# Optimization experiments

Hardware: AMD Instinct MI355X
Metric: run time of the kernel (lower is better)

The kernel has to match this reference:

```python
import jax, jax.numpy as jnp
import numpy as np

NUM_EMBEDDINGS = 512
EMBEDDING_DIM = 64
COMMITMENT_COST = 0.25


def setup_inputs() -> dict:
    key = jax.random.key(0)
    kx, kc = jax.random.split(key)
    x = jax.random.normal(kx, (32, 64, 64, EMBEDDING_DIM), dtype=jnp.float32)
    # nn.Embedding weight initialized uniform(-1/K, 1/K)
    codebook = jax.random.uniform(
        kc, (NUM_EMBEDDINGS, EMBEDDING_DIM), dtype=jnp.float32,
        minval=-1.0 / NUM_EMBEDDINGS, maxval=1.0 / NUM_EMBEDDINGS)
    return {"x": x, "codebook": codebook}


def reference(x, codebook):
    D = codebook.shape[1]
    flat = x.reshape(-1, D)  # [N, D]
    # squared euclidean distances; argmin is identical to cdist(p=2) argmin
    d2 = (jnp.sum(flat * flat, axis=-1, keepdims=True)
          - 2.0 * (flat @ codebook.T)
          + jnp.sum(codebook * codebook, axis=-1))  # [N, K]
    idx = jnp.argmin(d2, axis=1)  # [N]
    quantized = codebook[idx].reshape(x.shape)  # gather == one-hot @ codebook
    e_latent_loss = jnp.mean((jax.lax.stop_gradient(quantized) - x) ** 2)
    q_latent_loss = jnp.mean((quantized - jax.lax.stop_gradient(x)) ** 2)
    loss = q_latent_loss + COMMITMENT_COST * e_latent_loss
    # straight-through estimator
    quantized_st = x + jax.lax.stop_gradient(quantized - x)
    return quantized_st, loss
```

## Files before the change

kernel.cpp:

```cpp
#include <hip/hip_runtime.h>

#define DIMS 64
#define KCB 512
#define OUT_Q 8388608
#define MAIN_WGS 512

typedef float f32x4 __attribute__((ext_vector_type(4)));
typedef float f4    __attribute__((ext_vector_type(4)));
typedef short short8 __attribute__((ext_vector_type(8)));


static __device__ __forceinline__ unsigned int f2bf(float f) {
    unsigned int u = __float_as_uint(f);
    unsigned int r = u + 0x7FFFu + ((u >> 16) & 1u);
    return r >> 16;
}

__global__ void vq_prep(const float* __restrict__ cb, float* __restrict__ ws) {
    int t = blockIdx.x * blockDim.x + threadIdx.x;
    if (t < 4096) {
        int kt = t >> 7, rest = t & 127;
        int h = rest >> 6, l = rest & 63;
        int row = kt * 16 + (l & 15);
        int col = h * 32 + ((l >> 4) & 3) * 8;
        const f4* p = (const f4*)(cb + row * DIMS + col);
        f4 u0 = p[0], u1 = p[1];
        unsigned int* dst = (unsigned int*)((char*)ws + 4096 + kt * 2048 + h * 1024 + l * 16);
        dst[0] = (f2bf(u0[1]) << 16) | f2bf(u0[0]);
        dst[1] = (f2bf(u0[3]) << 16) | f2bf(u0[2]);
        dst[2] = (f2bf(u1[1]) << 16) | f2bf(u1[0]);
        dst[3] = (f2bf(u1[3]) << 16) | f2bf(u1[2]);
    } else if (t < 4096 + KCB) {
        int r = t - 4096;
        const f4* p = (const f4*)(cb + r * DIMS);
        float s = 0.0f;
#pragma unroll
        for (int i = 0; i < DIMS / 4; ++i) {
            f4 v = p[i];
            s += v[0]*v[0] + v[1]*v[1] + v[2]*v[2] + v[3]*v[3];
        }
        ws[512 + r] = -0.5f * s;
    }
}

__global__ __launch_bounds__(512, 4) void vq_main(const float* __restrict__ x,
                                                  const float* __restrict__ cb,
                                                  float* __restrict__ out,
                                                  float* __restrict__ ws) {
    __shared__ char lds[66560];

    const int tid  = threadIdx.x;
    const int lane = tid & 63;
    const int wid  = tid >> 6;
    const int wave = blockIdx.x * 8 + wid;
    const long rowbase = (long)wave * 32;
    const int r15 = lane & 15;
    const int g   = lane >> 4;

    {
        const f4* src = (const f4*)((const char*)ws + 4096);
        f4* ldsv = (f4*)lds;
#pragma unroll
        for (int r = 0; r < 8; ++r)
            ldsv[r * 512 + tid] = src[r * 512 + tid];
        ((float*)(lds + 65536))[tid] = ws[512 + tid];
    }

    short8 A00, A01, A10, A11;
    float xn0 = 0.0f, xn1 = 0.0f;
    {
        const float* xa = x + (rowbase + r15) * DIMS + g * 8;
#define LOADA(FR, OFF, XN)                                                     \
        {                                                                      \
            const f4* p_ = (const f4*)(xa + (OFF));                            \
            f4 a_ = p_[0], b_ = p_[1];                                         \
            XN += a_[0]*a_[0] + a_[1]*a_[1] + a_[2]*a_[2] + a_[3]*a_[3]        \
                + b_[0]*b_[0] + b_[1]*b_[1] + b_[2]*b_[2] + b_[3]*b_[3];       \
            union { unsigned int u[4]; short8 s; } q_;                         \
            asm("v_cvt_pk_bf16_f32 %0, %1, %2" : "=v"(q_.u[0]) : "v"(a_[0]), "v"(a_[1])); \
            asm("v_cvt_pk_bf16_f32 %0, %1, %2" : "=v"(q_.u[1]) : "v"(a_[2]), "v"(a_[3])); \
            asm("v_cvt_pk_bf16_f32 %0, %1, %2" : "=v"(q_.u[2]) : "v"(b_[0]), "v"(b_[1])); \
            asm("v_cvt_pk_bf16_f32 %0, %1, %2" : "=v"(q_.u[3]) : "v"(b_[2]), "v"(b_[3])); \
            FR = q_.s;                                                         \
        }
        LOADA(A00, 0, xn0)
        LOADA(A01, 32, xn0)
        LOADA(A10, 16 * DIMS, xn1)
        LOADA(A11, 16 * DIMS + 32, xn1)
#undef LOADA
    }
    xn0 += __shfl_xor(xn0, 16, 64);  xn0 += __shfl_xor(xn0, 32, 64);
    xn1 += __shfl_xor(xn1, 16, 64);  xn1 += __shfl_xor(xn1, 32, 64);

    __syncthreads();

    float bv00 = -3.4e38f, bv01 = -3.4e38f, bv02 = -3.4e38f, bv03 = -3.4e38f;
    float bv10 = -3.4e38f, bv11 = -3.4e38f, bv12 = -3.4e38f, bv13 = -3.4e38f;

    const char*  ldsb = lds;
    const float* ldsn = (const float*)(lds + 65536);
    const int laneoff = lane * 16;

#define PKMAX(BV, S)                                                           \
    BV = fmaxf(BV, __uint_as_float((__float_as_uint(S) & 0xFFFFFE00u) | kr));

#pragma unroll
    for (int kt = 0; kt < 32; ++kt) {
        short8 b0 = *(const short8*)(ldsb + kt * 2048 + laneoff);
        short8 b1 = *(const short8*)(ldsb + kt * 2048 + 1024 + laneoff);
        float ic = ldsn[kt * 16 + r15];
        f32x4 init = {ic, ic, ic, ic};
        f32x4 a0 = __builtin_amdgcn_mfma_f32_16x16x32_bf16(A00, b0, init, 0, 0, 0);
        a0       = __builtin_amdgcn_mfma_f32_16x16x32_bf16(A01, b1, a0,  0, 0, 0);
        f32x4 a1 = __builtin_amdgcn_mfma_f32_16x16x32_bf16(A10, b0, init, 0, 0, 0);
        a1       = __builtin_amdgcn_mfma_f32_16x16x32_bf16(A11, b1, a1,  0, 0, 0);
        const unsigned int kr = (unsigned int)(kt * 16 + r15);
        PKMAX(bv00, a0[0]) PKMAX(bv01, a0[1]) PKMAX(bv02, a0[2]) PKMAX(bv03, a0[3])
        PKMAX(bv10, a1[0]) PKMAX(bv11, a1[1]) PKMAX(bv12, a1[2]) PKMAX(bv13, a1[3])
    }
#undef PKMAX

#pragma unroll
    for (int st = 0; st < 4; ++st) {
        const int m = 1 << st;
        bv00 = fmaxf(bv00, __shfl_xor(bv00, m, 64));
        bv01 = fmaxf(bv01, __shfl_xor(bv01, m, 64));
        bv02 = fmaxf(bv02, __shfl_xor(bv02, m, 64));
        bv03 = fmaxf(bv03, __shfl_xor(bv03, m, 64));
        bv10 = fmaxf(bv10, __shfl_xor(bv10, m, 64));
        bv11 = fmaxf(bv11, __shfl_xor(bv11, m, 64));
        bv12 = fmaxf(bv12, __shfl_xor(bv12, m, 64));
        bv13 = fmaxf(bv13, __shfl_xor(bv13, m, 64));
    }

    const int orow = lane >> 2;
    const int cseg = lane & 3;
    const int j2   = orow & 3;
    int idx0 = (int)(__float_as_uint(j2 == 0 ? bv00 : j2 == 1 ? bv01 : j2 == 2 ? bv02 : bv03) & 511u);
    int idx1 = (int)(__float_as_uint(j2 == 0 ? bv10 : j2 == 1 ? bv11 : j2 == 2 ? bv12 : bv13) & 511u);

#define EPI(IDX, TOFF)                                                     \
    {                                                                      \
        const long row_ = rowbase + (TOFF) + orow;                         \
        const f4* cq_ = (const f4*)(cb + (long)(IDX) * DIMS + cseg * 16);  \
        f4* op_      = (f4*)(out + row_ * DIMS + cseg * 16);               \
        _Pragma("unroll")                                                  \
        for (int u = 0; u < 4; ++u) op_[u] = cq_[u];                       \
    }
    EPI(idx0, 0)
    EPI(idx1, 16)
#undef EPI

    float lsum = 0.0f;
    if (g == (r15 >> 2)) {
        const int jp = r15 & 3;
        float s0 = jp == 0 ? bv00 : jp == 1 ? bv01 : jp == 2 ? bv02 : bv03;
        float s1 = jp == 0 ? bv10 : jp == 1 ? bv11 : jp == 2 ? bv12 : bv13;
        s0 = __uint_as_float(__float_as_uint(s0) & 0xFFFFFE00u);
        s1 = __uint_as_float(__float_as_uint(s1) & 0xFFFFFE00u);
        lsum = (xn0 - 2.0f * s0) + (xn1 - 2.0f * s1);
    }
#pragma unroll
    for (int s = 0; s < 6; ++s) lsum += __shfl_xor(lsum, 1 << s, 64);

    __syncthreads();
    float* lsred = (float*)lds;
    if (lane == 0) lsred[wid] = lsum;
    __syncthreads();
    if (tid == 0) {
        ws[blockIdx.x] = lsred[0] + lsred[1] + lsred[2] + lsred[3]
                       + lsred[4] + lsred[5] + lsred[6] + lsred[7];
    }
}

__global__ __launch_bounds__(256) void vq_final(const float* __restrict__ ws,
                                                float* __restrict__ out) {
    const int t = threadIdx.x;
    float s = ws[t] + ws[t + 256];
#pragma unroll
    for (int st = 0; st < 6; ++st) s += __shfl_xor(s, 1 << st, 64);
    __shared__ float w2[4];
    if ((t & 63) == 0) w2[t >> 6] = s;
    __syncthreads();
    if (t == 0) {
        float total = w2[0] + w2[1] + w2[2] + w2[3];
        out[OUT_Q] = 1.25f * total / 8388608.0f;
    }
}

extern "C" void kernel_launch(void* const* d_in, const int* in_sizes, int n_in,
                              void* d_out, int out_size, void* d_ws, size_t ws_size,
                              hipStream_t stream) {
    const float* x  = (const float*)d_in[0];
    const float* cb = (const float*)d_in[1];
    float* out = (float*)d_out;
    float* ws  = (float*)d_ws;
    vq_prep<<<18, 256, 0, stream>>>(cb, ws);
    vq_main<<<MAIN_WGS, 512, 0, stream>>>(x, cb, out, ws);
    vq_final<<<1, 256, 0, stream>>>(ws, out);
}
```

Before: 31.53 us.

## Fuse codebook prep into main kernel and process 64 rows per wave

Drops the separate prep kernel. Each workgroup now converts the codebook to bf16 MFMA layout and computes its norms directly into LDS. Workgroups shrink to 256 threads, and each wave handles 64 rows with four MFMA tiles instead of two, so the grid stays at 512 blocks. This saves a launch and the workspace round trip, and gets more MFMA work out of each LDS B-fragment load. In exchange, every block redoes the codebook conversion from global memory, and register pressure rises.

```diff
diff --git a/kernel.cpp b/kernel.cpp
--- a/kernel.cpp
+++ b/kernel.cpp
@@ -3,7 +3,6 @@
 #define DIMS 64
 #define KCB 512
 #define OUT_Q 8388608
-#define MAIN_WGS 512
 
 typedef float f32x4 __attribute__((ext_vector_type(4)));
 typedef float f4    __attribute__((ext_vector_type(4)));
@@ -16,58 +15,22 @@
     return r >> 16;
 }
 
-__global__ void vq_prep(const float* __restrict__ cb, float* __restrict__ ws) {
-    int t = blockIdx.x * blockDim.x + threadIdx.x;
-    if (t < 4096) {
-        int kt = t >> 7, rest = t & 127;
-        int h = rest >> 6, l = rest & 63;
-        int row = kt * 16 + (l & 15);
-        int col = h * 32 + ((l >> 4) & 3) * 8;
-        const f4* p = (const f4*)(cb + row * DIMS + col);
-        f4 u0 = p[0], u1 = p[1];
-        unsigned int* dst = (unsigned int*)((char*)ws + 4096 + kt * 2048 + h * 1024 + l * 16);
-        dst[0] = (f2bf(u0[1]) << 16) | f2bf(u0[0]);
-        dst[1] = (f2bf(u0[3]) << 16) | f2bf(u0[2]);
-        dst[2] = (f2bf(u1[1]) << 16) | f2bf(u1[0]);
-        dst[3] = (f2bf(u1[3]) << 16) | f2bf(u1[2]);
-    } else if (t < 4096 + KCB) {
-        int r = t - 4096;
-        const f4* p = (const f4*)(cb + r * DIMS);
-        float s = 0.0f;
-#pragma unroll
-        for (int i = 0; i < DIMS / 4; ++i) {
-            f4 v = p[i];
-            s += v[0]*v[0] + v[1]*v[1] + v[2]*v[2] + v[3]*v[3];
-        }
-        ws[512 + r] = -0.5f * s;
-    }
-}
-
-__global__ __launch_bounds__(512, 4) void vq_main(const float* __restrict__ x,
+__global__ __launch_bounds__(256, 2) void vq_main(const float* __restrict__ x,
                                                   const float* __restrict__ cb,
                                                   float* __restrict__ out,
                                                   float* __restrict__ ws) {
-    __shared__ char lds[66560];
+    __shared__ f4 ldsv[4224];
 
     const int tid  = threadIdx.x;
     const int lane = tid & 63;
     const int wid  = tid >> 6;
-    const int wave = blockIdx.x * 8 + wid;
-    const long rowbase = (long)wave * 32;
+    const int wave = blockIdx.x * 4 + wid;
+    const long rowbase = (long)wave * 64;
     const int r15 = lane & 15;
     const int g   = lane >> 4;
 
-    {
-        const f4* src = (const f4*)((const char*)ws + 4096);
-        f4* ldsv = (f4*)lds;
-#pragma unroll
-        for (int r = 0; r < 8; ++r)
-            ldsv[r * 512 + tid] = src[r * 512 + tid];
-        ((float*)(lds + 65536))[tid] = ws[512 + tid];
-    }
-
-    short8 A00, A01, A10, A11;
-    float xn0 = 0.0f, xn1 = 0.0f;
+    short8 A00, A01, A10, A11, A20, A21, A30, A31;
+    float xn0 = 0.0f, xn1 = 0.0f, xn2 = 0.0f, xn3 = 0.0f;
     {
         const float* xa = x + (rowbase + r15) * DIMS + g * 8;
 #define LOADA(FR, OFF, XN)                                                     \
@@ -87,18 +50,58 @@
         LOADA(A01, 32, xn0)
         LOADA(A10, 16 * DIMS, xn1)
         LOADA(A11, 16 * DIMS + 32, xn1)
+        LOADA(A20, 32 * DIMS, xn2)
+        LOADA(A21, 32 * DIMS + 32, xn2)
+        LOADA(A30, 48 * DIMS, xn3)
+        LOADA(A31, 48 * DIMS + 32, xn3)
 #undef LOADA
     }
     xn0 += __shfl_xor(xn0, 16, 64);  xn0 += __shfl_xor(xn0, 32, 64);
     xn1 += __shfl_xor(xn1, 16, 64);  xn1 += __shfl_xor(xn1, 32, 64);
+    xn2 += __shfl_xor(xn2, 16, 64);  xn2 += __shfl_xor(xn2, 32, 64);
+    xn3 += __shfl_xor(xn3, 16, 64);  xn3 += __shfl_xor(xn3, 32, 64);
+
+    {
+#pragma unroll
+        for (int i = 0; i < 16; ++i) {
+            const int s = tid + i * 256;
+            const int kt = s >> 7, rest = s & 127;
+            const int h = rest >> 6, l = rest & 63;
+            const int row = kt * 16 + (l & 15);
+            const int col = h * 32 + ((l >> 4) & 3) * 8;
+            const f4* p = (const f4*)(cb + row * DIMS + col);
+            f4 u0 = p[0], u1 = p[1];
+            union { unsigned int u[4]; f4 f; } q;
+            q.u[0] = (f2bf(u0[1]) << 16) | f2bf(u0[0]);
+            q.u[1] = (f2bf(u0[3]) << 16) | f2bf(u0[2]);
+            q.u[2] = (f2bf(u1[1]) << 16) | f2bf(u1[0]);
+            q.u[3] = (f2bf(u1[3]) << 16) | f2bf(u1[2]);
+            ldsv[s] = q.f;
+        }
+        float* ldsn_w = (float*)ldsv + 16384;
+#pragma unroll
+        for (int rr = 0; rr < 2; ++rr) {
+            const int r = tid + rr * 256;
+            const f4* p = (const f4*)(cb + r * DIMS);
+            float s0 = 0.0f;
+#pragma unroll
+            for (int i = 0; i < 16; ++i) {
+                f4 v = p[i];
+                s0 += v[0]*v[0] + v[1]*v[1] + v[2]*v[2] + v[3]*v[3];
+            }
+            ldsn_w[r] = -0.5f * s0;
+        }
+    }
 
     __syncthreads();
 
     float bv00 = -3.4e38f, bv01 = -3.4e38f, bv02 = -3.4e38f, bv03 = -3.4e38f;
     float bv10 = -3.4e38f, bv11 = -3.4e38f, bv12 = -3.4e38f, bv13 = -3.4e38f;
-
-    const char*  ldsb = lds;
-    const float* ldsn = (const float*)(lds + 65536);
+    float bv20 = -3.4e38f, bv21 = -3.4e38f, bv22 = -3.4e38f, bv23 = -3.4e38f;
+    float bv30 = -3.4e38f, bv31 = -3.4e38f, bv32 = -3.4e38f, bv33 = -3.4e38f;
+
+    const char*  ldsb = (const char*)ldsv;
+    const float* ldsn = (const float*)ldsv + 16384;
     const int laneoff = lane * 16;
 
 #define PKMAX(BV, S)                                                           \
@@ -114,9 +117,15 @@
         a0       = __builtin_amdgcn_mfma_f32_16x16x32_bf16(A01, b1, a0,  0, 0, 0);
         f32x4 a1 = __builtin_amdgcn_mfma_f32_16x16x32_bf16(A10, b0, init, 0, 0, 0);
         a1       = __builtin_amdgcn_mfma_f32_16x16x32_bf16(A11, b1, a1,  0, 0, 0);
+        f32x4 a2 = __builtin_amdgcn_mfma_f32_16x16x32_bf16(A20, b0, init, 0, 0, 0);
+        a2       = __builtin_amdgcn_mfma_f32_16x16x32_bf16(A21, b1, a2,  0, 0, 0);
+        f32x4 a3 = __builtin_amdgcn_mfma_f32_16x16x32_bf16(A30, b0, init, 0, 0, 0);
+        a3       = __builtin_amdgcn_mfma_f32_16x16x32_bf16(A31, b1, a3,  0, 0, 0);
         const unsigned int kr = (unsigned int)(kt * 16 + r15);
         PKMAX(bv00, a0[0]) PKMAX(bv01, a0[1]) PKMAX(bv02, a0[2]) PKMAX(bv03, a0[3])
         PKMAX(bv10, a1[0]) PKMAX(bv11, a1[1]) PKMAX(bv12, a1[2]) PKMAX(bv13, a1[3])
+        PKMAX(bv20, a2[0]) PKMAX(bv21, a2[1]) PKMAX(bv22, a2[2]) PKMAX(bv23, a2[3])
+        PKMAX(bv30, a3[0]) PKMAX(bv31, a3[1]) PKMAX(bv32, a3[2]) PKMAX(bv33, a3[3])
     }
 #undef PKMAX
 
@@ -131,13 +140,26 @@
         bv11 = fmaxf(bv11, __shfl_xor(bv11, m, 64));
         bv12 = fmaxf(bv12, __shfl_xor(bv12, m, 64));
         bv13 = fmaxf(bv13, __shfl_xor(bv13, m, 64));
+        bv20 = fmaxf(bv20, __shfl_xor(bv20, m, 64));
+        bv21 = fmaxf(bv21, __shfl_xor(bv21, m, 64));
+        bv22 = fmaxf(bv22, __shfl_xor(bv22, m, 64));
+        bv23 = fmaxf(bv23, __shfl_xor(bv23, m, 64));
+        bv30 = fmaxf(bv30, __shfl_xor(bv30, m, 64));
+        bv31 = fmaxf(bv31, __shfl_xor(bv31, m, 64));
+        bv32 = fmaxf(bv32, __shfl_xor(bv32, m, 64));
+        bv33 = fmaxf(bv33, __shfl_xor(bv33, m, 64));
     }
 
     const int orow = lane >> 2;
     const int cseg = lane & 3;
     const int j2   = orow & 3;
-    int idx0 = (int)(__float_as_uint(j2 == 0 ? bv00 : j2 == 1 ? bv01 : j2 == 2 ? bv02 : bv03) & 511u);
-    int idx1 = (int)(__float_as_uint(j2 == 0 ? bv10 : j2 == 1 ? bv11 : j2 == 2 ? bv12 : bv13) & 511u);
+#define SEL(T) (int)(__float_as_uint(j2 == 0 ? bv##T##0 : j2 == 1 ? bv##T##1 : \
+                                     j2 == 2 ? bv##T##2 : bv##T##3) & 511u)
+    const int idx0 = SEL(0);
+    const int idx1 = SEL(1);
+    const int idx2 = SEL(2);
+    const int idx3 = SEL(3);
+#undef SEL
 
 #define EPI(IDX, TOFF)                                                     \
     {                                                                      \
@@ -149,27 +171,28 @@
     }
     EPI(idx0, 0)
     EPI(idx1, 16)
+    EPI(idx2, 32)
+    EPI(idx3, 48)
 #undef EPI
 
     float lsum = 0.0f;
     if (g == (r15 >> 2)) {
         const int jp = r15 & 3;
-        float s0 = jp == 0 ? bv00 : jp == 1 ? bv01 : jp == 2 ? bv02 : bv03;
-        float s1 = jp == 0 ? bv10 : jp == 1 ? bv11 : jp == 2 ? bv12 : bv13;
-        s0 = __uint_as_float(__float_as_uint(s0) & 0xFFFFFE00u);
-        s1 = __uint_as_float(__float_as_uint(s1) & 0xFFFFFE00u);
-        lsum = (xn0 - 2.0f * s0) + (xn1 - 2.0f * s1);
+#define SSEL(T) __uint_as_float(__float_as_uint(jp == 0 ? bv##T##0 : jp == 1 ? bv##T##1 : \
+                                jp == 2 ? bv##T##2 : bv##T##3) & 0xFFFFFE00u)
+        lsum = (xn0 - 2.0f * SSEL(0)) + (xn1 - 2.0f * SSEL(1))
+             + (xn2 - 2.0f * SSEL(2)) + (xn3 - 2.0f * SSEL(3));
+#undef SSEL
     }
 #pragma unroll
     for (int s = 0; s < 6; ++s) lsum += __shfl_xor(lsum, 1 << s, 64);
 
     __syncthreads();
-    float* lsred = (float*)lds;
+    float* lsred = (float*)ldsv;
     if (lane == 0) lsred[wid] = lsum;
     __syncthreads();
     if (tid == 0) {
-        ws[blockIdx.x] = lsred[0] + lsred[1] + lsred[2] + lsred[3]
-                       + lsred[4] + lsred[5] + lsred[6] + lsred[7];
+        ws[blockIdx.x] = lsred[0] + lsred[1] + lsred[2] + lsred[3];
     }
 }
 
@@ -195,7 +218,6 @@
     const float* cb = (const float*)d_in[1];
     float* out = (float*)d_out;
     float* ws  = (float*)d_ws;
-    vq_prep<<<18, 256, 0, stream>>>(cb, ws);
-    vq_main<<<MAIN_WGS, 512, 0, stream>>>(x, cb, out, ws);
+    vq_main<<<512, 256, 0, stream>>>(x, cb, out, ws);
     vq_final<<<1, 256, 0, stream>>>(ws, out);
 }
```

New measurement: 42.77 us. +35.6%, slower.

## Fuse codebook prep into main kernel, building bf16 tiles in LDS per block

Applied to the files above, without the earlier changes.

Drops the separate prep kernel that converted the codebook to a bf16 MFMA layout and computed the norms. Each workgroup of the main kernel now reads the fp32 codebook, converts it and computes the norms straight into LDS, which removes one launch and the round trip through the workspace. In exchange every one of the 512 blocks repeats the conversion and norm work (extra ALU and L2 reads of the codebook). The occupancy hint moves to the waves-per-EU attribute.

```diff
diff --git a/kernel.cpp b/kernel.cpp
--- a/kernel.cpp
+++ b/kernel.cpp
@@ -16,38 +16,13 @@
     return r >> 16;
 }
 
-__global__ void vq_prep(const float* __restrict__ cb, float* __restrict__ ws) {
-    int t = blockIdx.x * blockDim.x + threadIdx.x;
-    if (t < 4096) {
-        int kt = t >> 7, rest = t & 127;
-        int h = rest >> 6, l = rest & 63;
-        int row = kt * 16 + (l & 15);
-        int col = h * 32 + ((l >> 4) & 3) * 8;
-        const f4* p = (const f4*)(cb + row * DIMS + col);
-        f4 u0 = p[0], u1 = p[1];
-        unsigned int* dst = (unsigned int*)((char*)ws + 4096 + kt * 2048 + h * 1024 + l * 16);
-        dst[0] = (f2bf(u0[1]) << 16) | f2bf(u0[0]);
-        dst[1] = (f2bf(u0[3]) << 16) | f2bf(u0[2]);
-        dst[2] = (f2bf(u1[1]) << 16) | f2bf(u1[0]);
-        dst[3] = (f2bf(u1[3]) << 16) | f2bf(u1[2]);
-    } else if (t < 4096 + KCB) {
-        int r = t - 4096;
-        const f4* p = (const f4*)(cb + r * DIMS);
-        float s = 0.0f;
-#pragma unroll
-        for (int i = 0; i < DIMS / 4; ++i) {
-            f4 v = p[i];
-            s += v[0]*v[0] + v[1]*v[1] + v[2]*v[2] + v[3]*v[3];
-        }
-        ws[512 + r] = -0.5f * s;
-    }
-}
-
-__global__ __launch_bounds__(512, 4) void vq_main(const float* __restrict__ x,
-                                                  const float* __restrict__ cb,
-                                                  float* __restrict__ out,
-                                                  float* __restrict__ ws) {
-    __shared__ char lds[66560];
+__global__ __launch_bounds__(512)
+__attribute__((amdgpu_waves_per_eu(4, 4)))
+void vq_main(const float* __restrict__ x,
+             const float* __restrict__ cb,
+             float* __restrict__ out,
+             float* __restrict__ ws) {
+    __shared__ f4 ldsv[4224];
 
     const int tid  = threadIdx.x;
     const int lane = tid & 63;
@@ -56,15 +31,6 @@
     const long rowbase = (long)wave * 32;
     const int r15 = lane & 15;
     const int g   = lane >> 4;
-
-    {
-        const f4* src = (const f4*)((const char*)ws + 4096);
-        f4* ldsv = (f4*)lds;
-#pragma unroll
-        for (int r = 0; r < 8; ++r)
-            ldsv[r * 512 + tid] = src[r * 512 + tid];
-        ((float*)(lds + 65536))[tid] = ws[512 + tid];
-    }
 
     short8 A00, A01, A10, A11;
     float xn0 = 0.0f, xn1 = 0.0f;
@@ -92,13 +58,41 @@
     xn0 += __shfl_xor(xn0, 16, 64);  xn0 += __shfl_xor(xn0, 32, 64);
     xn1 += __shfl_xor(xn1, 16, 64);  xn1 += __shfl_xor(xn1, 32, 64);
 
+    {
+#pragma unroll
+        for (int i = 0; i < 8; ++i) {
+            const int s = tid + i * 512;
+            const int kt = s >> 7, rest = s & 127;
+            const int h = rest >> 6, l = rest & 63;
+            const int row = kt * 16 + (l & 15);
+            const int col = h * 32 + ((l >> 4) & 3) * 8;
+            const f4* p = (const f4*)(cb + row * DIMS + col);
+            f4 u0 = p[0], u1 = p[1];
+            union { unsigned int u[4]; f4 f; } q;
+            q.u[0] = (f2bf(u0[1]) << 16) | f2bf(u0[0]);
+            q.u[1] = (f2bf(u0[3]) << 16) | f2bf(u0[2]);
+            q.u[2] = (f2bf(u1[1]) << 16) | f2bf(u1[0]);
+            q.u[3] = (f2bf(u1[3]) << 16) | f2bf(u1[2]);
+            ldsv[s] = q.f;
+        }
+        float* ldsn_w = (float*)ldsv + 16384;
+        const f4* p = (const f4*)(cb + tid * DIMS);
+        float s0 = 0.0f;
+#pragma unroll
+        for (int i = 0; i < 16; ++i) {
+            f4 v = p[i];
+            s0 += v[0]*v[0] + v[1]*v[1] + v[2]*v[2] + v[3]*v[3];
+        }
+        ldsn_w[tid] = -0.5f * s0;
+    }
+
     __syncthreads();
 
     float bv00 = -3.4e38f, bv01 = -3.4e38f, bv02 = -3.4e38f, bv03 = -3.4e38f;
     float bv10 = -3.4e38f, bv11 = -3.4e38f, bv12 = -3.4e38f, bv13 = -3.4e38f;
 
-    const char*  ldsb = lds;
-    const float* ldsn = (const float*)(lds + 65536);
+    const char*  ldsb = (const char*)ldsv;
+    const float* ldsn = (const float*)ldsv + 16384;
     const int laneoff = lane * 16;
 
 #define PKMAX(BV, S)                                                           \
@@ -154,17 +148,16 @@
     float lsum = 0.0f;
     if (g == (r15 >> 2)) {
         const int jp = r15 & 3;
-        float s0 = jp == 0 ? bv00 : jp == 1 ? bv01 : jp == 2 ? bv02 : bv03;
-        float s1 = jp == 0 ? bv10 : jp == 1 ? bv11 : jp == 2 ? bv12 : bv13;
-        s0 = __uint_as_float(__float_as_uint(s0) & 0xFFFFFE00u);
-        s1 = __uint_as_float(__float_as_uint(s1) & 0xFFFFFE00u);
-        lsum = (xn0 - 2.0f * s0) + (xn1 - 2.0f * s1);
+#define SSEL(T) __uint_as_float(__float_as_uint(jp == 0 ? bv##T##0 : jp == 1 ? bv##T##1 : \
+                                jp == 2 ? bv##T##2 : bv##T##3) & 0xFFFFFE00u)
+        lsum = (xn0 - 2.0f * SSEL(0)) + (xn1 - 2.0f * SSEL(1));
+#undef SSEL
     }
 #pragma unroll
     for (int s = 0; s < 6; ++s) lsum += __shfl_xor(lsum, 1 << s, 64);
 
     __syncthreads();
-    float* lsred = (float*)lds;
+    float* lsred = (float*)ldsv;
     if (lane == 0) lsred[wid] = lsum;
     __syncthreads();
     if (tid == 0) {
@@ -195,7 +188,6 @@
     const float* cb = (const float*)d_in[1];
     float* out = (float*)d_out;
     float* ws  = (float*)d_ws;
-    vq_prep<<<18, 256, 0, stream>>>(cb, ws);
     vq_main<<<MAIN_WGS, 512, 0, stream>>>(x, cb, out, ws);
     vq_final<<<1, 256, 0, stream>>>(ws, out);
 }
```

Result: slower. 40.99 us (+30.0%).

## Switch distance GEMM to FP8 MFMA and halve rows per wave

Applied to the files above, without the earlier changes.

The codebook is pre-quantized to FP8 with a scale of 256 and x is converted with v_cvt_pk_fp8_f32, so the distance matmul runs on 16x16x32 fp8 MFMA instead of bf16. This halves the LDS footprint of the codebook. Each wave now handles 16 rows instead of 32, with 1024 workgroups and launch bounds raised for higher occupancy, and the final reduction is widened to match. FP8 precision in the argmin can select different codebook entries than the fp32 reference, so the results risk mismatches in the indices and the loss.

```diff
diff --git a/kernel.cpp b/kernel.cpp
--- a/kernel.cpp
+++ b/kernel.cpp
@@ -3,17 +3,37 @@
 #define DIMS 64
 #define KCB 512
 #define OUT_Q 8388608
-#define MAIN_WGS 512
+#define MAIN_WGS 1024
 
 typedef float f32x4 __attribute__((ext_vector_type(4)));
 typedef float f4    __attribute__((ext_vector_type(4)));
-typedef short short8 __attribute__((ext_vector_type(8)));
-
-
-static __device__ __forceinline__ unsigned int f2bf(float f) {
+
+
+static __device__ __forceinline__ unsigned int f2fp8(float f) {
     unsigned int u = __float_as_uint(f);
-    unsigned int r = u + 0x7FFFu + ((u >> 16) & 1u);
-    return r >> 16;
+    unsigned int sign = (u >> 24) & 0x80u;
+    if ((u & 0x7FFFFFFFu) == 0) return sign;
+    int exp = (int)((u >> 23) & 0xFFu) - 127;
+    unsigned int m24 = (u & 0x7FFFFFu) | 0x800000u;
+    if (exp >= -6) {
+        unsigned int keep = m24 >> 20;
+        unsigned int rem = m24 & 0xFFFFFu;
+        if (rem > 0x80000u || (rem == 0x80000u && (keep & 1u))) keep++;
+        if (keep >= 16u) { keep >>= 1; exp++; }
+        int e = exp + 7;
+        if (e >= 16) return sign | 0x7Eu;
+        if (e == 15 && (keep & 7u) == 7u) return sign | 0x7Eu;
+        return sign | ((unsigned)e << 3) | (keep & 7u);
+    } else {
+        int sh = 14 - exp;
+        if (sh > 31) return sign;
+        unsigned int keep = m24 >> sh;
+        unsigned int rem = m24 & ((1u << sh) - 1u);
+        unsigned int half = 1u << (sh - 1);
+        if (rem > half || (rem == half && (keep & 1u))) keep++;
+        if (keep >= 8u) return sign | 0x08u;
+        return sign | keep;
+    }
 }
 
 __global__ void vq_prep(const float* __restrict__ cb, float* __restrict__ ws) {
@@ -25,11 +45,17 @@
         int col = h * 32 + ((l >> 4) & 3) * 8;
         const f4* p = (const f4*)(cb + row * DIMS + col);
         f4 u0 = p[0], u1 = p[1];
-        unsigned int* dst = (unsigned int*)((char*)ws + 4096 + kt * 2048 + h * 1024 + l * 16);
-        dst[0] = (f2bf(u0[1]) << 16) | f2bf(u0[0]);
-        dst[1] = (f2bf(u0[3]) << 16) | f2bf(u0[2]);
-        dst[2] = (f2bf(u1[1]) << 16) | f2bf(u1[0]);
-        dst[3] = (f2bf(u1[3]) << 16) | f2bf(u1[2]);
+        unsigned int lo = f2fp8(256.0f * u0[0])
+                        | (f2fp8(256.0f * u0[1]) << 8)
+                        | (f2fp8(256.0f * u0[2]) << 16)
+                        | (f2fp8(256.0f * u0[3]) << 24);
+        unsigned int hi = f2fp8(256.0f * u1[0])
+                        | (f2fp8(256.0f * u1[1]) << 8)
+                        | (f2fp8(256.0f * u1[2]) << 16)
+                        | (f2fp8(256.0f * u1[3]) << 24);
+        unsigned int* dst = (unsigned int*)((char*)ws + 8192 + kt * 1024 + h * 512 + l * 8);
+        dst[0] = lo;
+        dst[1] = hi;
     } else if (t < 4096 + KCB) {
         int r = t - 4096;
         const f4* p = (const f4*)(cb + r * DIMS);
@@ -39,126 +65,118 @@
             f4 v = p[i];
             s += v[0]*v[0] + v[1]*v[1] + v[2]*v[2] + v[3]*v[3];
         }
-        ws[512 + r] = -0.5f * s;
-    }
-}
-
-__global__ __launch_bounds__(512, 4) void vq_main(const float* __restrict__ x,
+        ((float*)((char*)ws + 4096))[r] = -128.0f * s;
+    }
+}
+
+__global__ __launch_bounds__(512, 8) void vq_main(const float* __restrict__ x,
                                                   const float* __restrict__ cb,
                                                   float* __restrict__ out,
                                                   float* __restrict__ ws) {
-    __shared__ char lds[66560];
+    __shared__ char lds[34816];
 
     const int tid  = threadIdx.x;
     const int lane = tid & 63;
     const int wid  = tid >> 6;
-    const int wave = blockIdx.x * 8 + wid;
-    const long rowbase = (long)wave * 32;
+    const long rowbase = ((long)blockIdx.x * 8 + wid) * 16;
     const int r15 = lane & 15;
     const int g   = lane >> 4;
 
     {
-        const f4* src = (const f4*)((const char*)ws + 4096);
-        f4* ldsv = (f4*)lds;
-#pragma unroll
-        for (int r = 0; r < 8; ++r)
-            ldsv[r * 512 + tid] = src[r * 512 + tid];
-        ((float*)(lds + 65536))[tid] = ws[512 + tid];
-    }
-
-    short8 A00, A01, A10, A11;
-    float xn0 = 0.0f, xn1 = 0.0f;
+        const f4* src = (const f4*)((const char*)ws + 8192);
+        f4 s0 = src[tid];
+        f4 s1 = src[512 + tid];
+        f4 s2 = src[1024 + tid];
+        f4 s3 = src[1536 + tid];
+        float nv = ((const float*)((const char*)ws + 4096))[tid];
+        f4* dst = (f4*)lds;
+        dst[tid]        = s0;
+        dst[512 + tid]  = s1;
+        dst[1024 + tid] = s2;
+        dst[1536 + tid] = s3;
+        ((float*)(lds + 32768))[tid] = nv;
+    }
+
+    unsigned long A0, A1;
+    float xn0;
     {
         const float* xa = x + (rowbase + r15) * DIMS + g * 8;
-#define LOADA(FR, OFF, XN)                                                     \
-        {                                                                      \
-            const f4* p_ = (const f4*)(xa + (OFF));                            \
-            f4 a_ = p_[0], b_ = p_[1];                                         \
-            XN += a_[0]*a_[0] + a_[1]*a_[1] + a_[2]*a_[2] + a_[3]*a_[3]        \
-                + b_[0]*b_[0] + b_[1]*b_[1] + b_[2]*b_[2] + b_[3]*b_[3];       \
-            union { unsigned int u[4]; short8 s; } q_;                         \
-            asm("v_cvt_pk_bf16_f32 %0, %1, %2" : "=v"(q_.u[0]) : "v"(a_[0]), "v"(a_[1])); \
-            asm("v_cvt_pk_bf16_f32 %0, %1, %2" : "=v"(q_.u[1]) : "v"(a_[2]), "v"(a_[3])); \
-            asm("v_cvt_pk_bf16_f32 %0, %1, %2" : "=v"(q_.u[2]) : "v"(b_[0]), "v"(b_[1])); \
-            asm("v_cvt_pk_bf16_f32 %0, %1, %2" : "=v"(q_.u[3]) : "v"(b_[2]), "v"(b_[3])); \
-            FR = q_.s;                                                         \
-        }
-        LOADA(A00, 0, xn0)
-        LOADA(A01, 32, xn0)
-        LOADA(A10, 16 * DIMS, xn1)
-        LOADA(A11, 16 * DIMS + 32, xn1)
-#undef LOADA
-    }
-    xn0 += __shfl_xor(xn0, 16, 64);  xn0 += __shfl_xor(xn0, 32, 64);
-    xn1 += __shfl_xor(xn1, 16, 64);  xn1 += __shfl_xor(xn1, 32, 64);
-
-    __syncthreads();
-
-    float bv00 = -3.4e38f, bv01 = -3.4e38f, bv02 = -3.4e38f, bv03 = -3.4e38f;
-    float bv10 = -3.4e38f, bv11 = -3.4e38f, bv12 = -3.4e38f, bv13 = -3.4e38f;
+        f4 a0 = *(const f4*)(xa);
+        f4 a1 = *(const f4*)(xa + 4);
+        f4 a2 = *(const f4*)(xa + 32);
+        f4 a3 = *(const f4*)(xa + 36);
+        xn0 = a0[0]*a0[0]+a0[1]*a0[1]+a0[2]*a0[2]+a0[3]*a0[3]
+            + a1[0]*a1[0]+a1[1]*a1[1]+a1[2]*a1[2]+a1[3]*a1[3]
+            + a2[0]*a2[0]+a2[1]*a2[1]+a2[2]*a2[2]+a2[3]*a2[3]
+            + a3[0]*a3[0]+a3[1]*a3[1]+a3[2]*a3[2]+a3[3]*a3[3];
+        unsigned int t0, t1, t2, t3, t4, t5, t6, t7;
+        asm("v_cvt_pk_fp8_f32 %0, %1, %2" : "=v"(t0) : "v"(a0[0]), "v"(a0[1]));
+        asm("v_cvt_pk_fp8_f32 %0, %1, %2" : "=v"(t1) : "v"(a0[2]), "v"(a0[3]));
+        asm("v_cvt_pk_fp8_f32 %0, %1, %2" : "=v"(t2) : "v"(a1[0]), "v"(a1[1]));
+        asm("v_cvt_pk_fp8_f32 %0, %1, %2" : "=v"(t3) : "v"(a1[2]), "v"(a1[3]));
+        asm("v_cvt_pk_fp8_f32 %0, %1, %2" : "=v"(t4) : "v"(a2[0]), "v"(a2[1]));
+        asm("v_cvt_pk_fp8_f32 %0, %1, %2" : "=v"(t5) : "v"(a2[2]), "v"(a2[3]));
+        asm("v_cvt_pk_fp8_f32 %0, %1, %2" : "=v"(t6) : "v"(a3[0]), "v"(a3[1]));
+        asm("v_cvt_pk_fp8_f32 %0, %1, %2" : "=v"(t7) : "v"(a3[2]), "v"(a3[3]));
+        unsigned int dw0 = (t0 & 0xFFFFu) | (t1 << 16);
+        unsigned int dw1 = (t2 & 0xFFFFu) | (t3 << 16);
+        unsigned int dw2 = (t4 & 0xFFFFu) | (t5 << 16);
+        unsigned int dw3 = (t6 & 0xFFFFu) | (t7 << 16);
+        A0 = (unsigned long)dw0 | ((unsigned long)dw1 << 32);
+        A1 = (unsigned long)dw2 | ((unsigned long)dw3 << 32);
+    }
+    xn0 += __shfl_xor(xn0, 16, 64);
+    xn0 += __shfl_xor(xn0, 32, 64);
+
+    __syncthreads();
+
+    float bv0 = -3.4e38f, bv1 = -3.4e38f, bv2 = -3.4e38f, bv3 = -3.4e38f;
 
     const char*  ldsb = lds;
-    const float* ldsn = (const float*)(lds + 65536);
-    const int laneoff = lane * 16;
-
-#define PKMAX(BV, S)                                                           \
-    BV = fmaxf(BV, __uint_as_float((__float_as_uint(S) & 0xFFFFFE00u) | kr));
+    const float* ldsn = (const float*)(lds + 32768);
+    const int laneoff = lane * 8;
 
 #pragma unroll
     for (int kt = 0; kt < 32; ++kt) {
-        short8 b0 = *(const short8*)(ldsb + kt * 2048 + laneoff);
-        short8 b1 = *(const short8*)(ldsb + kt * 2048 + 1024 + laneoff);
+        unsigned long b0 = *(const unsigned long*)(ldsb + kt * 1024 + laneoff);
+        unsigned long b1 = *(const unsigned long*)(ldsb + kt * 1024 + 512 + laneoff);
         float ic = ldsn[kt * 16 + r15];
         f32x4 init = {ic, ic, ic, ic};
-        f32x4 a0 = __builtin_amdgcn_mfma_f32_16x16x32_bf16(A00, b0, init, 0, 0, 0);
-        a0       = __builtin_amdgcn_mfma_f32_16x16x32_bf16(A01, b1, a0,  0, 0, 0);
-        f32x4 a1 = __builtin_amdgcn_mfma_f32_16x16x32_bf16(A10, b0, init, 0, 0, 0);
-        a1       = __builtin_amdgcn_mfma_f32_16x16x32_bf16(A11, b1, a1,  0, 0, 0);
+        f32x4 q = __builtin_amdgcn_mfma_f32_16x16x32_fp8_fp8((long)A0, (long)b0, init, 0, 0, 0);
+        q       = __builtin_amdgcn_mfma_f32_16x16x32_fp8_fp8((long)A1, (long)b1, q,    0, 0, 0);
         const unsigned int kr = (unsigned int)(kt * 16 + r15);
-        PKMAX(bv00, a0[0]) PKMAX(bv01, a0[1]) PKMAX(bv02, a0[2]) PKMAX(bv03, a0[3])
-        PKMAX(bv10, a1[0]) PKMAX(bv11, a1[1]) PKMAX(bv12, a1[2]) PKMAX(bv13, a1[3])
-    }
-#undef PKMAX
+        bv0 = fmaxf(bv0, __uint_as_float((__float_as_uint(q[0]) & 0xFFFFFE00u) | kr));
+        bv1 = fmaxf(bv1, __uint_as_float((__float_as_uint(q[1]) & 0xFFFFFE00u) | kr));
+        bv2 = fmaxf(bv2, __uint_as_float((__float_as_uint(q[2]) & 0xFFFFFE00u) | kr));
+        bv3 = fmaxf(bv3, __uint_as_float((__float_as_uint(q[3]) & 0xFFFFFE00u) | kr));
+    }
 
 #pragma unroll
     for (int st = 0; st < 4; ++st) {
         const int m = 1 << st;
-        bv00 = fmaxf(bv00, __shfl_xor(bv00, m, 64));
-        bv01 = fmaxf(bv01, __shfl_xor(bv01, m, 64));
-        bv02 = fmaxf(bv02, __shfl_xor(bv02, m, 64));
-        bv03 = fmaxf(bv03, __shfl_xor(bv03, m, 64));
-        bv10 = fmaxf(bv10, __shfl_xor(bv10, m, 64));
-        bv11 = fmaxf(bv11, __shfl_xor(bv11, m, 64));
-        bv12 = fmaxf(bv12, __shfl_xor(bv12, m, 64));
-        bv13 = fmaxf(bv13, __shfl_xor(bv13, m, 64));
-    }
-
-    const int orow = lane >> 2;
-    const int cseg = lane & 3;
-    const int j2   = orow & 3;
-    int idx0 = (int)(__float_as_uint(j2 == 0 ? bv00 : j2 == 1 ? bv01 : j2 == 2 ? bv02 : bv03) & 511u);
-    int idx1 = (int)(__float_as_uint(j2 == 0 ? bv10 : j2 == 1 ? bv11 : j2 == 2 ? bv12 : bv13) & 511u);
-
-#define EPI(IDX, TOFF)                                                     \
-    {                                                                      \
-        const long row_ = rowbase + (TOFF) + orow;                         \
-        const f4* cq_ = (const f4*)(cb + (long)(IDX) * DIMS + cseg * 16);  \
-        f4* op_      = (f4*)(out + row_ * DIMS + cseg * 16);               \
-        _Pragma("unroll")                                                  \
-        for (int u = 0; u < 4; ++u) op_[u] = cq_[u];                       \
-    }
-    EPI(idx0, 0)
-    EPI(idx1, 16)
-#undef EPI
+        bv0 = fmaxf(bv0, __shfl_xor(bv0, m, 64));
+        bv1 = fmaxf(bv1, __shfl_xor(bv1, m, 64));
+        bv2 = fmaxf(bv2, __shfl_xor(bv2, m, 64));
+        bv3 = fmaxf(bv3, __shfl_xor(bv3, m, 64));
+    }
+
+    {
+        const int orow = lane >> 2;
+        const int cseg = lane & 3;
+        const int j2   = orow & 3;
+        const int idx = (int)(__float_as_uint(j2 == 0 ? bv0 : j2 == 1 ? bv1 :
+                                              j2 == 2 ? bv2 : bv3) & 511u);
+        const f4* cq = (const f4*)(cb + (long)idx * DIMS + cseg * 16);
+        f4* op = (f4*)(out + (rowbase + orow) * DIMS + cseg * 16);
+        op[0] = cq[0]; op[1] = cq[1]; op[2] = cq[2]; op[3] = cq[3];
+    }
 
     float lsum = 0.0f;
     if (g == (r15 >> 2)) {
         const int jp = r15 & 3;
-        float s0 = jp == 0 ? bv00 : jp == 1 ? bv01 : jp == 2 ? bv02 : bv03;
-        float s1 = jp == 0 ? bv10 : jp == 1 ? bv11 : jp == 2 ? bv12 : bv13;
+        float s0 = jp == 0 ? bv0 : jp == 1 ? bv1 : jp == 2 ? bv2 : bv3;
         s0 = __uint_as_float(__float_as_uint(s0) & 0xFFFFFE00u);
-        s1 = __uint_as_float(__float_as_uint(s1) & 0xFFFFFE00u);
-        lsum = (xn0 - 2.0f * s0) + (xn1 - 2.0f * s1);
+        lsum = xn0 - s0 * 0.0078125f;
     }
 #pragma unroll
     for (int s = 0; s < 6; ++s) lsum += __shfl_xor(lsum, 1 << s, 64);
@@ -176,7 +194,7 @@
 __global__ __launch_bounds__(256) void vq_final(const float* __restrict__ ws,
                                                 float* __restrict__ out) {
     const int t = threadIdx.x;
-    float s = ws[t] + ws[t + 256];
+    float s = ws[t] + ws[t + 256] + ws[t + 512] + ws[t + 768];
 #pragma unroll
     for (int st = 0; st < 6; ++st) s += __shfl_xor(s, 1 << st, 64);
     __shared__ float w2[4];
```

Result: no change. 31.44 us (-0.3%).
